# Performance work log

Hardware: AMD Instinct MI355X
Metric: run time of the kernel (lower is better)

## Reference

```python
import jax, jax.numpy as jnp
import numpy as np

B, T, IN, H = 256, 512, 19, 512  # batch, seq_len, input_size, hidden_size
OUT = 1


def setup_inputs() -> dict:
    key = jax.random.key(0)
    ks = jax.random.split(key, 16)
    std = 1.0 / np.sqrt(H)  # reset_parameters: uniform(-1/sqrt(H), 1/sqrt(H))
    u = lambda k, shape: jax.random.uniform(k, shape, jnp.float32, -std, std)
    return {
        "input": jax.random.normal(ks[0], (B, T, IN), jnp.float32),
        "l1_Wx": u(ks[1], (4 * H, IN)),
        "l1_bx": u(ks[2], (4 * H,)),
        "l1_Wh": u(ks[3], (4 * H, H)),
        "l1_bh": u(ks[4], (4 * H,)),
        "l2_Wx": u(ks[5], (4 * H, H)),
        "l2_bx": u(ks[6], (4 * H,)),
        "l2_Wh": u(ks[7], (4 * H, H)),
        "l2_bh": u(ks[8], (4 * H,)),
        "fc1_W": u(ks[9], (H // 2, H)),
        "fc1_b": u(ks[10], (H // 2,)),
        "fc2_W": u(ks[11], (H // 4, H // 2)),
        "fc2_b": u(ks[12], (H // 4,)),
        "fc3_W": u(ks[13], (OUT, H // 4)),
        "fc3_b": u(ks[14], (OUT,)),
    }


def _lstm_layer(x, Wx, bx, Wh, bh):
    # Precompute the input projection for all timesteps (identical math to
    # per-step xh(input), but one big GEMM). x: [B, T, in] -> pre: [B, T, 4H]
    pre = jnp.einsum('bti,gi->btg', x, Wx) + bx
    h_dim = Wh.shape[1]

    def step(carry, p_t):
        h, c = carry
        gates = p_t + h @ Wh.T + bh  # [B, 4H]
        i, f, g, o = jnp.split(gates, 4, axis=-1)
        c = jax.nn.sigmoid(f) * c + jax.nn.sigmoid(i) * jnp.tanh(g)
        h = jax.nn.sigmoid(o) * jnp.tanh(c)
        return (h, c), h

    h0 = jnp.zeros((x.shape[0], h_dim), x.dtype)
    _, hs = jax.lax.scan(step, (h0, h0), jnp.swapaxes(pre, 0, 1))  # hs: [T, B, H]
    return jnp.swapaxes(hs, 0, 1)  # [B, T, H]


def reference(input, l1_Wx, l1_bx, l1_Wh, l1_bh, l2_Wx, l2_bx, l2_Wh, l2_bh,
              fc1_W, fc1_b, fc2_W, fc2_b, fc3_W, fc3_b):
    h1 = _lstm_layer(input, l1_Wx, l1_bx, l1_Wh, l1_bh)
    h2 = _lstm_layer(h1, l2_Wx, l2_bx, l2_Wh, l2_bh)
    out = h2[:, -1, :]  # last timestep of top layer
    out = jax.nn.relu(out @ fc1_W.T + fc1_b)  # dropout = identity (inference)
    out = jax.nn.relu(out @ fc2_W.T + fc2_b)
    out = out @ fc3_W.T + fc3_b
    return jnp.squeeze(out)  # [B]
```

## Files before the change

kernel.cpp:

```cpp
#include <hip/hip_runtime.h>
#include <hip/hip_cooperative_groups.h>

namespace cg = cooperative_groups;

#define Bb   256
#define Tt   512
#define INx  19
#define Hh   512
#define NWG  256
#define NTHR 512

#define PART_FLOATS (8 * 12 * 256)
#define WX1_FLOATS  (8 * 20)
#define FCB_FLOATS  (Hh + 256 + 128)
#define SMEM_FLOATS (PART_FLOATS + WX1_FLOATS + FCB_FLOATS)
#define SMEM_BYTES  (SMEM_FLOATS * 4)

typedef unsigned int u32;
typedef unsigned long long u64;

__device__ __forceinline__ float sigf(float x) { return 1.0f / (1.0f + __expf(-x)); }
__device__ __forceinline__ float tanhfast(float x) {
    float e = __expf(2.0f * x);
    return 1.0f - 2.0f / (e + 1.0f);
}

union pcast { u64 u; float2 f; };
__device__ __forceinline__ void gstore2(float2* p, float2 v) {
    pcast c; c.f = v;
    __hip_atomic_store((u64*)p, c.u, __ATOMIC_RELAXED, __HIP_MEMORY_SCOPE_AGENT);
}

__device__ __forceinline__ void gbar(u32* flags, int wgid, int tid, u32 phase) {
    __syncthreads();
    if (tid == 0)
        __hip_atomic_store(&flags[wgid], phase, __ATOMIC_RELEASE, __HIP_MEMORY_SCOPE_AGENT);
    if (tid < NWG) {
        const u32* fp = &flags[tid];
        while (__hip_atomic_load(fp, __ATOMIC_RELAXED, __HIP_MEMORY_SCOPE_AGENT) < phase)
            __builtin_amdgcn_s_sleep(2);
    }
    __syncthreads();
    __builtin_amdgcn_fence(__ATOMIC_ACQUIRE, "agent");
}

__device__ __forceinline__ void ldh(const float4* __restrict__ hp, int c,
                                    float4 (&A)[4], float4 (&B)[4]) {
    #pragma unroll
    for (int kk = 0; kk < 4; ++kk) {
        A[kk] = hp[(size_t)(c * 4 + kk) * 128];
        B[kk] = hp[(size_t)(c * 4 + kk) * 128 + 1];
    }
}

__device__ __forceinline__ void fmac(const float4 (&A)[4], const float4 (&B)[4],
                                     const float* const (&wb1)[4],
                                     const float* const (&wb2)[4],
                                     const float* const (&wb3)[4], int c4,
                                     float (&a1)[4][4], float (&ax)[4][4], float (&ah)[4][4]) {
    #pragma unroll
    for (int g = 0; g < 4; ++g) {
        const float4 w1 = *reinterpret_cast<const float4*>(wb1[g] + c4);
        const float4 w2 = *reinterpret_cast<const float4*>(wb2[g] + c4);
        const float4 w3 = *reinterpret_cast<const float4*>(wb3[g] + c4);
        a1[g][0] += A[0].x*w1.x + A[1].x*w1.y + A[2].x*w1.z + A[3].x*w1.w;
        a1[g][1] += A[0].z*w1.x + A[1].z*w1.y + A[2].z*w1.z + A[3].z*w1.w;
        a1[g][2] += B[0].x*w1.x + B[1].x*w1.y + B[2].x*w1.z + B[3].x*w1.w;
        a1[g][3] += B[0].z*w1.x + B[1].z*w1.y + B[2].z*w1.z + B[3].z*w1.w;
        ax[g][0] += A[0].x*w2.x + A[1].x*w2.y + A[2].x*w2.z + A[3].x*w2.w;
        ax[g][1] += A[0].z*w2.x + A[1].z*w2.y + A[2].z*w2.z + A[3].z*w2.w;
        ax[g][2] += B[0].x*w2.x + B[1].x*w2.y + B[2].x*w2.z + B[3].x*w2.w;
        ax[g][3] += B[0].z*w2.x + B[1].z*w2.y + B[2].z*w2.z + B[3].z*w2.w;
        ah[g][0] += A[0].y*w3.x + A[1].y*w3.y + A[2].y*w3.z + A[3].y*w3.w;
        ah[g][1] += A[0].w*w3.x + A[1].w*w3.y + A[2].w*w3.z + A[3].w*w3.w;
        ah[g][2] += B[0].y*w3.x + B[1].y*w3.y + B[2].y*w3.z + B[3].y*w3.w;
        ah[g][3] += B[0].w*w3.x + B[1].w*w3.y + B[2].w*w3.z + B[3].w*w3.w;
    }
}

__global__ void __launch_bounds__(NTHR, 2)
lstm_fused(const float* __restrict__ input,
           const float* __restrict__ l1_Wx, const float* __restrict__ l1_bx,
           const float* __restrict__ l1_Wh, const float* __restrict__ l1_bh,
           const float* __restrict__ l2_Wx, const float* __restrict__ l2_bx,
           const float* __restrict__ l2_Wh, const float* __restrict__ l2_bh,
           const float* __restrict__ fc1_W, const float* __restrict__ fc1_b,
           const float* __restrict__ fc2_W, const float* __restrict__ fc2_b,
           const float* __restrict__ fc3_W, const float* __restrict__ fc3_b,
           float* __restrict__ out, float* __restrict__ ws)
{
    extern __shared__ float smem[];
    float* part = smem;
    float* wx1l = smem + PART_FLOATS;
    float* fcb  = wx1l + WX1_FLOATS;

    cg::grid_group grid = cg::this_grid();
    const int wgid = blockIdx.x;
    const int jb = wgid * 2;
    const int tid = threadIdx.x;

    const int wu = __builtin_amdgcn_readfirstlane(tid >> 6);
    const int su = wu & 1;
    const int kq = wu >> 1;
    const int bg = tid & 63;
    const int su2 = tid >> 8;
    const int fb  = tid & 255;
    const int j2  = jb + su2;

    float2* PA = (float2*)ws;
    float2* PB = PA + Hh * Bb;
    u32* flags = (u32*)(PB + Hh * Bb);

    if (tid == 0)
        __hip_atomic_store(&flags[wgid], 0u, __ATOMIC_RELAXED, __HIP_MEMORY_SCOPE_AGENT);
    grid.sync();

    const float* wb1[4]; const float* wb2[4]; const float* wb3[4];
    {
        const int j = jb + su;
        #pragma unroll
        for (int g = 0; g < 4; ++g) {
            const size_t off = (size_t)(g * Hh + j) * Hh + kq * 128;
            wb1[g] = l1_Wh + off;
            wb2[g] = l2_Wx + off;
            wb3[g] = l2_Wh + off;
        }
    }

    if (tid < 8 * INx) {
        const int r = tid / INx, i = tid - r * INx;
        const int u = r >> 2, g = r & 3;
        wx1l[r * 20 + i] = l1_Wx[(size_t)(g * Hh + jb + u) * INx + i];
    }
    float b1r[4], b2r[4];
    #pragma unroll
    for (int g = 0; g < 4; ++g) {
        const int row = g * Hh + j2;
        b1r[g] = l1_bx[row] + l1_bh[row];
        b2r[g] = l2_bx[row] + l2_bh[row];
    }
    __syncthreads();

    float c1 = 0.f, c2 = 0.f;
    {
        const float* xr = input + (size_t)fb * Tt * INx;
        float s[4];
        #pragma unroll
        for (int g = 0; g < 4; ++g) {
            float acc = b1r[g];
            #pragma unroll
            for (int i = 0; i < INx; ++i) acc += xr[i] * wx1l[(su2 * 4 + g) * 20 + i];
            s[g] = acc;
        }
        c1 = sigf(s[0]) * tanhfast(s[2]);
        gstore2(&PA[(size_t)j2 * Bb + fb], make_float2(sigf(s[3]) * tanhfast(c1), 0.f));
    }
    gbar(flags, wgid, tid, 1u);

    const float2* Pc = PA; float2* Pn = PB;
    const int blk = su * 4 + kq;

    for (int t = 0; t < Tt; ++t) {
        const bool doL1 = (t < Tt - 1);

        float a1[4][4], ax[4][4], ah[4][4];
        #pragma unroll
        for (int g = 0; g < 4; ++g)
            #pragma unroll
            for (int b = 0; b < 4; ++b) { a1[g][b] = 0.f; ax[g][b] = 0.f; ah[g][b] = 0.f; }

        const float4* hp = (const float4*)Pc + (size_t)(kq * 128) * 128 + bg * 2;

        float4 E0[4], E1[4], O0[4], O1[4];
        ldh(hp, 0, E0, E1);
        #pragma unroll 1
        for (int c = 0; c < 32; c += 2) {
            ldh(hp, c + 1, O0, O1);
            fmac(E0, E1, wb1, wb2, wb3, (c    ) * 4, a1, ax, ah);
            if (c < 30) ldh(hp, c + 2, E0, E1);
            fmac(O0, O1, wb1, wb2, wb3, (c + 1) * 4, a1, ax, ah);
        }

        {
            float* pw = part + (size_t)(blk * 12) * 256 + bg * 4;
            #pragma unroll
            for (int g = 0; g < 4; ++g) {
                *reinterpret_cast<float4*>(pw + (0 + g) * 256) = make_float4(a1[g][0], a1[g][1], a1[g][2], a1[g][3]);
                *reinterpret_cast<float4*>(pw + (4 + g) * 256) = make_float4(ax[g][0], ax[g][1], ax[g][2], ax[g][3]);
                *reinterpret_cast<float4*>(pw + (8 + g) * 256) = make_float4(ah[g][0], ah[g][1], ah[g][2], ah[g][3]);
            }
        }
        __syncthreads();

        {
            float s1[4], s2[4];
            #pragma unroll
            for (int g = 0; g < 4; ++g) {
                float A1 = 0.f, AX = 0.f, AH = 0.f;
                #pragma unroll
                for (int q = 0; q < 4; ++q) {
                    const float* pr = part + (size_t)((su2 * 4 + q) * 12) * 256 + fb;
                    A1 += pr[(0 + g) * 256];
                    AX += pr[(4 + g) * 256];
                    AH += pr[(8 + g) * 256];
                }
                s1[g] = A1 + b1r[g];
                s2[g] = AX + AH + b2r[g];
            }
            float h1v = 0.f;
            if (doL1) {
                const float* xr = input + ((size_t)fb * Tt + t + 1) * INx;
                #pragma unroll
                for (int g = 0; g < 4; ++g) {
                    float acc = s1[g];
                    #pragma unroll
                    for (int i = 0; i < INx; ++i) acc += xr[i] * wx1l[(su2 * 4 + g) * 20 + i];
                    s1[g] = acc;
                }
                const float ig = sigf(s1[0]), fg = sigf(s1[1]);
                const float gg = tanhfast(s1[2]), og = sigf(s1[3]);
                c1 = fg * c1 + ig * gg;
                h1v = og * tanhfast(c1);
            }
            const float ig = sigf(s2[0]), fg = sigf(s2[1]);
            const float gg = tanhfast(s2[2]), og = sigf(s2[3]);
            c2 = fg * c2 + ig * gg;
            gstore2(&Pn[(size_t)j2 * Bb + fb], make_float2(h1v, og * tanhfast(c2)));
        }

        gbar(flags, wgid, tid, (u32)(t + 2));

        const float2* tp = Pc; Pc = Pn; Pn = (float2*)tp;
    }

    float* hh  = fcb;
    float* a1s = fcb + Hh;
    float* a2s = fcb + Hh + 256;
    hh[tid] = Pc[(size_t)tid * Bb + wgid].y;
    __syncthreads();
    if (tid < 256) {
        float acc = fc1_b[tid];
        const float* wr = fc1_W + (size_t)tid * Hh;
        for (int i = 0; i < Hh; ++i) acc += wr[i] * hh[i];
        a1s[tid] = fmaxf(acc, 0.0f);
    }
    __syncthreads();
    if (tid < 128) {
        float acc = fc2_b[tid];
        const float* wr = fc2_W + (size_t)tid * 256;
        for (int i = 0; i < 256; ++i) acc += wr[i] * a1s[i];
        a2s[tid] = fmaxf(acc, 0.0f);
    }
    __syncthreads();
    if (tid == 0) {
        float acc = fc3_b[0];
        for (int i = 0; i < 128; ++i) acc += fc3_W[i] * a2s[i];
        out[wgid] = acc;
    }
}

extern "C" void kernel_launch(void* const* d_in, const int* in_sizes, int n_in,
                              void* d_out, int out_size, void* d_ws, size_t ws_size,
                              hipStream_t stream)
{
    (void)in_sizes; (void)n_in; (void)out_size; (void)ws_size;

    const float* input = (const float*)d_in[0];
    const float* l1_Wx = (const float*)d_in[1];
    const float* l1_bx = (const float*)d_in[2];
    const float* l1_Wh = (const float*)d_in[3];
    const float* l1_bh = (const float*)d_in[4];
    const float* l2_Wx = (const float*)d_in[5];
    const float* l2_bx = (const float*)d_in[6];
    const float* l2_Wh = (const float*)d_in[7];
    const float* l2_bh = (const float*)d_in[8];
    const float* fc1_W = (const float*)d_in[9];
    const float* fc1_b = (const float*)d_in[10];
    const float* fc2_W = (const float*)d_in[11];
    const float* fc2_b = (const float*)d_in[12];
    const float* fc3_W = (const float*)d_in[13];
    const float* fc3_b = (const float*)d_in[14];
    float* out = (float*)d_out;
    float* ws  = (float*)d_ws;

    hipFuncSetAttribute((const void*)lstm_fused,
                        hipFuncAttributeMaxDynamicSharedMemorySize, SMEM_BYTES);

    void* args[] = {
        &input,
        &l1_Wx, &l1_bx, &l1_Wh, &l1_bh,
        &l2_Wx, &l2_bx, &l2_Wh, &l2_bh,
        &fc1_W, &fc1_b, &fc2_W, &fc2_b, &fc3_W, &fc3_b,
        &out, &ws
    };
    hipLaunchCooperativeKernel((void*)lstm_fused, dim3(NWG), dim3(NTHR), args,
                               SMEM_BYTES, stream);
}
```

Before: 29.86 ms.

## Repartition work to 4 hidden units × 128 batch per workgroup with deeper prefetch

Each workgroup now owns 4 hidden units for one half of the batch instead of 2 units for the whole batch. This halves the per-wave batch tile and splits the K dimension into 2 chunks instead of 4, so the cross-wave shared-memory reduction shrinks. The h-vector loads use a 4-deep software prefetch ring, and the next-step input x row is loaded before the barrier to hide its latency. The grid-barrier acquire fence now runs on one wave only, followed by an extra __syncthreads. Each weight load now feeds fewer batch columns, so weight traffic per FLOP rises, and the h tile each workgroup reads changes shape.

Measured after the change: 68.83 ms. 2.31x slower.

```diff
diff --git a/kernel.cpp b/kernel.cpp
--- a/kernel.cpp
+++ b/kernel.cpp
@@ -10,8 +10,8 @@
 #define NWG  256
 #define NTHR 512
 
-#define PART_FLOATS (8 * 12 * 256)
-#define WX1_FLOATS  (8 * 20)
+#define PART_FLOATS (8 * 12 * 128)
+#define WX1_FLOATS  (16 * 20)
 #define FCB_FLOATS  (Hh + 256 + 128)
 #define SMEM_FLOATS (PART_FLOATS + WX1_FLOATS + FCB_FLOATS)
 #define SMEM_BYTES  (SMEM_FLOATS * 4)
@@ -41,40 +41,34 @@
             __builtin_amdgcn_s_sleep(2);
     }
     __syncthreads();
-    __builtin_amdgcn_fence(__ATOMIC_ACQUIRE, "agent");
-}
-
-__device__ __forceinline__ void ldh(const float4* __restrict__ hp, int c,
-                                    float4 (&A)[4], float4 (&B)[4]) {
+    if (tid < 64)
+        __builtin_amdgcn_fence(__ATOMIC_ACQUIRE, "agent");
+    __syncthreads();
+}
+
+__device__ __forceinline__ void ldc(const float4* __restrict__ hp, int c,
+                                    float4 (&H)[4]) {
     #pragma unroll
-    for (int kk = 0; kk < 4; ++kk) {
-        A[kk] = hp[(size_t)(c * 4 + kk) * 128];
-        B[kk] = hp[(size_t)(c * 4 + kk) * 128 + 1];
-    }
-}
-
-__device__ __forceinline__ void fmac(const float4 (&A)[4], const float4 (&B)[4],
+    for (int kk = 0; kk < 4; ++kk)
+        H[kk] = hp[(size_t)c * 512 + (size_t)kk * 128];
+}
+
+__device__ __forceinline__ void fmac(const float4 (&H)[4],
                                      const float* const (&wb1)[4],
                                      const float* const (&wb2)[4],
-                                     const float* const (&wb3)[4], int c4,
-                                     float (&a1)[4][4], float (&ax)[4][4], float (&ah)[4][4]) {
+                                     const float* const (&wb3)[4], int koff,
+                                     float (&a1)[4][2], float (&ax)[4][2], float (&ah)[4][2]) {
     #pragma unroll
     for (int g = 0; g < 4; ++g) {
-        const float4 w1 = *reinterpret_cast<const float4*>(wb1[g] + c4);
-        const float4 w2 = *reinterpret_cast<const float4*>(wb2[g] + c4);
-        const float4 w3 = *reinterpret_cast<const float4*>(wb3[g] + c4);
-        a1[g][0] += A[0].x*w1.x + A[1].x*w1.y + A[2].x*w1.z + A[3].x*w1.w;
-        a1[g][1] += A[0].z*w1.x + A[1].z*w1.y + A[2].z*w1.z + A[3].z*w1.w;
-        a1[g][2] += B[0].x*w1.x + B[1].x*w1.y + B[2].x*w1.z + B[3].x*w1.w;
-        a1[g][3] += B[0].z*w1.x + B[1].z*w1.y + B[2].z*w1.z + B[3].z*w1.w;
-        ax[g][0] += A[0].x*w2.x + A[1].x*w2.y + A[2].x*w2.z + A[3].x*w2.w;
-        ax[g][1] += A[0].z*w2.x + A[1].z*w2.y + A[2].z*w2.z + A[3].z*w2.w;
-        ax[g][2] += B[0].x*w2.x + B[1].x*w2.y + B[2].x*w2.z + B[3].x*w2.w;
-        ax[g][3] += B[0].z*w2.x + B[1].z*w2.y + B[2].z*w2.z + B[3].z*w2.w;
-        ah[g][0] += A[0].y*w3.x + A[1].y*w3.y + A[2].y*w3.z + A[3].y*w3.w;
-        ah[g][1] += A[0].w*w3.x + A[1].w*w3.y + A[2].w*w3.z + A[3].w*w3.w;
-        ah[g][2] += B[0].y*w3.x + B[1].y*w3.y + B[2].y*w3.z + B[3].y*w3.w;
-        ah[g][3] += B[0].w*w3.x + B[1].w*w3.y + B[2].w*w3.z + B[3].w*w3.w;
+        const float4 w1 = *reinterpret_cast<const float4*>(wb1[g] + koff);
+        const float4 w2 = *reinterpret_cast<const float4*>(wb2[g] + koff);
+        const float4 w3 = *reinterpret_cast<const float4*>(wb3[g] + koff);
+        a1[g][0] += H[0].x*w1.x + H[1].x*w1.y + H[2].x*w1.z + H[3].x*w1.w;
+        a1[g][1] += H[0].z*w1.x + H[1].z*w1.y + H[2].z*w1.z + H[3].z*w1.w;
+        ax[g][0] += H[0].x*w2.x + H[1].x*w2.y + H[2].x*w2.z + H[3].x*w2.w;
+        ax[g][1] += H[0].z*w2.x + H[1].z*w2.y + H[2].z*w2.z + H[3].z*w2.w;
+        ah[g][0] += H[0].y*w3.x + H[1].y*w3.y + H[2].y*w3.z + H[3].y*w3.w;
+        ah[g][1] += H[0].w*w3.x + H[1].w*w3.y + H[2].w*w3.z + H[3].w*w3.w;
     }
 }
 
@@ -96,16 +90,20 @@
 
     cg::grid_group grid = cg::this_grid();
     const int wgid = blockIdx.x;
-    const int jb = wgid * 2;
+    const int ug = wgid >> 1;
+    const int bs = wgid & 1;
+    const int jb = ug * 4;
     const int tid = threadIdx.x;
 
-    const int wu = __builtin_amdgcn_readfirstlane(tid >> 6);
-    const int su = wu & 1;
-    const int kq = wu >> 1;
+    const int wid = __builtin_amdgcn_readfirstlane(tid >> 6);
+    const int su = wid >> 1;
+    const int kq = wid & 1;
     const int bg = tid & 63;
-    const int su2 = tid >> 8;
-    const int fb  = tid & 255;
-    const int j2  = jb + su2;
+    const int b0 = bs * 128 + bg * 2;
+    const int fu = tid >> 7;
+    const int fb = tid & 127;
+    const int bx = bs * 128 + fb;
+    const int j2 = jb + fu;
 
     float2* PA = (float2*)ws;
     float2* PB = PA + Hh * Bb;
@@ -120,14 +118,14 @@
         const int j = jb + su;
         #pragma unroll
         for (int g = 0; g < 4; ++g) {
-            const size_t off = (size_t)(g * Hh + j) * Hh + kq * 128;
+            const size_t off = (size_t)(g * Hh + j) * Hh + kq * 256;
             wb1[g] = l1_Wh + off;
             wb2[g] = l2_Wx + off;
             wb3[g] = l2_Wh + off;
         }
     }
 
-    if (tid < 8 * INx) {
+    if (tid < 16 * INx) {
         const int r = tid / INx, i = tid - r * INx;
         const int u = r >> 2, g = r & 3;
         wx1l[r * 20 + i] = l1_Wx[(size_t)(g * Hh + jb + u) * INx + i];
@@ -143,52 +141,62 @@
 
     float c1 = 0.f, c2 = 0.f;
     {
-        const float* xr = input + (size_t)fb * Tt * INx;
+        const float* xr = input + (size_t)bx * Tt * INx;
         float s[4];
         #pragma unroll
         for (int g = 0; g < 4; ++g) {
             float acc = b1r[g];
             #pragma unroll
-            for (int i = 0; i < INx; ++i) acc += xr[i] * wx1l[(su2 * 4 + g) * 20 + i];
+            for (int i = 0; i < INx; ++i) acc += xr[i] * wx1l[(fu * 4 + g) * 20 + i];
             s[g] = acc;
         }
         c1 = sigf(s[0]) * tanhfast(s[2]);
-        gstore2(&PA[(size_t)j2 * Bb + fb], make_float2(sigf(s[3]) * tanhfast(c1), 0.f));
+        gstore2(&PA[(size_t)j2 * Bb + bx], make_float2(sigf(s[3]) * tanhfast(c1), 0.f));
     }
     gbar(flags, wgid, tid, 1u);
 
     const float2* Pc = PA; float2* Pn = PB;
-    const int blk = su * 4 + kq;
 
     for (int t = 0; t < Tt; ++t) {
         const bool doL1 = (t < Tt - 1);
 
-        float a1[4][4], ax[4][4], ah[4][4];
+        float a1[4][2], ax[4][2], ah[4][2];
         #pragma unroll
         for (int g = 0; g < 4; ++g)
             #pragma unroll
-            for (int b = 0; b < 4; ++b) { a1[g][b] = 0.f; ax[g][b] = 0.f; ah[g][b] = 0.f; }
-
-        const float4* hp = (const float4*)Pc + (size_t)(kq * 128) * 128 + bg * 2;
-
-        float4 E0[4], E1[4], O0[4], O1[4];
-        ldh(hp, 0, E0, E1);
+            for (int b = 0; b < 2; ++b) { a1[g][b] = 0.f; ax[g][b] = 0.f; ah[g][b] = 0.f; }
+
+        const float4* hp = (const float4*)Pc + (size_t)(kq * 256) * 128 + (b0 >> 1);
+
+        float4 B0[4], B1[4], B2[4], B3[4];
+        ldc(hp, 0, B0); ldc(hp, 1, B1); ldc(hp, 2, B2); ldc(hp, 3, B3);
         #pragma unroll 1
-        for (int c = 0; c < 32; c += 2) {
-            ldh(hp, c + 1, O0, O1);
-            fmac(E0, E1, wb1, wb2, wb3, (c    ) * 4, a1, ax, ah);
-            if (c < 30) ldh(hp, c + 2, E0, E1);
-            fmac(O0, O1, wb1, wb2, wb3, (c + 1) * 4, a1, ax, ah);
-        }
+        for (int c = 0; c < 60; c += 4) {
+            fmac(B0, wb1, wb2, wb3, (c + 0) * 4, a1, ax, ah); ldc(hp, c + 4, B0);
+            fmac(B1, wb1, wb2, wb3, (c + 1) * 4, a1, ax, ah); ldc(hp, c + 5, B1);
+            fmac(B2, wb1, wb2, wb3, (c + 2) * 4, a1, ax, ah); ldc(hp, c + 6, B2);
+            fmac(B3, wb1, wb2, wb3, (c + 3) * 4, a1, ax, ah); ldc(hp, c + 7, B3);
+        }
+        fmac(B0, wb1, wb2, wb3, 240, a1, ax, ah);
+        fmac(B1, wb1, wb2, wb3, 244, a1, ax, ah);
+        fmac(B2, wb1, wb2, wb3, 248, a1, ax, ah);
+        fmac(B3, wb1, wb2, wb3, 252, a1, ax, ah);
 
         {
-            float* pw = part + (size_t)(blk * 12) * 256 + bg * 4;
+            float* pw = part + (size_t)(wid * 12) * 128 + bg * 2;
             #pragma unroll
             for (int g = 0; g < 4; ++g) {
-                *reinterpret_cast<float4*>(pw + (0 + g) * 256) = make_float4(a1[g][0], a1[g][1], a1[g][2], a1[g][3]);
-                *reinterpret_cast<float4*>(pw + (4 + g) * 256) = make_float4(ax[g][0], ax[g][1], ax[g][2], ax[g][3]);
-                *reinterpret_cast<float4*>(pw + (8 + g) * 256) = make_float4(ah[g][0], ah[g][1], ah[g][2], ah[g][3]);
+                *reinterpret_cast<float2*>(pw + (0 + g) * 128) = make_float2(a1[g][0], a1[g][1]);
+                *reinterpret_cast<float2*>(pw + (4 + g) * 128) = make_float2(ax[g][0], ax[g][1]);
+                *reinterpret_cast<float2*>(pw + (8 + g) * 128) = make_float2(ah[g][0], ah[g][1]);
             }
+        }
+
+        float xv[INx];
+        if (doL1) {
+            const float* xr = input + ((size_t)bx * Tt + t + 1) * INx;
+            #pragma unroll
+            for (int i = 0; i < INx; ++i) xv[i] = xr[i];
         }
         __syncthreads();
 
@@ -196,25 +204,19 @@
             float s1[4], s2[4];
             #pragma unroll
             for (int g = 0; g < 4; ++g) {
-                float A1 = 0.f, AX = 0.f, AH = 0.f;
-                #pragma unroll
-                for (int q = 0; q < 4; ++q) {
-                    const float* pr = part + (size_t)((su2 * 4 + q) * 12) * 256 + fb;
-                    A1 += pr[(0 + g) * 256];
-                    AX += pr[(4 + g) * 256];
-                    AH += pr[(8 + g) * 256];
-                }
-                s1[g] = A1 + b1r[g];
-                s2[g] = AX + AH + b2r[g];
+                const float* p0 = part + (size_t)((fu * 2 + 0) * 12) * 128 + fb;
+                const float* p1 = part + (size_t)((fu * 2 + 1) * 12) * 128 + fb;
+                s1[g] = p0[(0 + g) * 128] + p1[(0 + g) * 128] + b1r[g];
+                s2[g] = p0[(4 + g) * 128] + p1[(4 + g) * 128]
+                      + p0[(8 + g) * 128] + p1[(8 + g) * 128] + b2r[g];
             }
             float h1v = 0.f;
             if (doL1) {
-                const float* xr = input + ((size_t)fb * Tt + t + 1) * INx;
                 #pragma unroll
                 for (int g = 0; g < 4; ++g) {
                     float acc = s1[g];
                     #pragma unroll
-                    for (int i = 0; i < INx; ++i) acc += xr[i] * wx1l[(su2 * 4 + g) * 20 + i];
+                    for (int i = 0; i < INx; ++i) acc += xv[i] * wx1l[(fu * 4 + g) * 20 + i];
                     s1[g] = acc;
                 }
                 const float ig = sigf(s1[0]), fg = sigf(s1[1]);
@@ -225,7 +227,7 @@
             const float ig = sigf(s2[0]), fg = sigf(s2[1]);
             const float gg = tanhfast(s2[2]), og = sigf(s2[3]);
             c2 = fg * c2 + ig * gg;
-            gstore2(&Pn[(size_t)j2 * Bb + fb], make_float2(h1v, og * tanhfast(c2)));
+            gstore2(&Pn[(size_t)j2 * Bb + bx], make_float2(h1v, og * tanhfast(c2)));
         }
 
         gbar(flags, wgid, tid, (u32)(t + 2));
```
